# Kernel tuning notes

Hardware: AMD Instinct MI355X
Metric: run time of the kernel (lower is better)

Reference implementation:

```python
import jax, jax.numpy as jnp
import numpy as np

MOMENTUM = 0.5  # ODCMemory momentum
EPS = 1e-10

L, D, C, B = 500000, 256, 1024, 16384  # bank length, feat_dim, num_classes, batch


def setup_inputs() -> dict:
    key = jax.random.key(0)
    k0, k1, k2, k3, k4 = jax.random.split(key, 5)
    feature_bank = jax.random.normal(k0, (L, D), dtype=jnp.float32)
    # bank is stored L2-normalized (init_memory normalizes before copy)
    feature_bank = feature_bank / (jnp.linalg.norm(feature_bank, axis=1, keepdims=True) + EPS)
    label_bank = jax.random.randint(k1, (L,), 0, C, dtype=jnp.int64)
    centroids = jax.random.normal(k2, (C, D), dtype=jnp.float32)
    ind = jax.random.randint(k3, (B,), 0, L, dtype=jnp.int64)
    feature = jax.random.normal(k4, (B, D), dtype=jnp.float32)
    return {"feature_bank": feature_bank, "label_bank": label_bank,
            "centroids": centroids, "ind": ind, "feature": feature}


def reference(feature_bank, label_bank, centroids, ind, feature):
    """ODCMemory.update_samples_memory: gather -> momentum-normalize -> centroid
    similarity argmax -> scatter back. Returns (new_bank, new_labels, change_ratio)."""
    # normalize incoming batch features
    feat_n = feature / (jnp.linalg.norm(feature, axis=1, keepdims=True) + EPS)  # [B, D]
    # gather old features, momentum update, re-normalize
    feat_old = feature_bank[ind]                                               # [B, D]
    feat_new = (1.0 - MOMENTUM) * feat_old + MOMENTUM * feat_n
    feat_new = feat_new / (jnp.linalg.norm(feat_new, axis=1, keepdims=True) + EPS)
    # scatter updated features back into the bank
    new_bank = feature_bank.at[ind].set(feat_new)                              # [L, D]
    # similarity to centroids and relabel
    sim = jnp.einsum('cd,bd->cb', centroids, feat_new)                         # [C, B]
    newlabel = jnp.argmax(sim, axis=0).astype(label_bank.dtype)                # [B]
    old_label = label_bank[ind]
    change_ratio = jnp.mean((newlabel != old_label).astype(jnp.float32))
    new_labels = label_bank.at[ind].set(newlabel)
    return new_bank, new_labels, change_ratio
```

## Files before the change

kernel.cpp:

```cpp
#include <hip/hip_runtime.h>
#include <math.h>


constexpr int Lb = 500000;
constexpr int Dm = 256;
constexpr int D4 = 64;
constexpr int Cc = 1024;
constexpr int Bb = 16384;
constexpr float EPSV = 1e-10f;

constexpr int ROWS  = 8;
constexpr int GCLS  = Bb / ROWS;
constexpr int GCPY  = 2048;
constexpr int GMAIN = GCLS + GCPY;
constexpr int GMARK = Bb / 256;
constexpr int GPRE  = 1024;
constexpr int GPOST = 1024;

typedef float vfloat4 __attribute__((ext_vector_type(4)));

__device__ __forceinline__ float wave_sum64(float v) {
#pragma unroll
  for (int off = 32; off > 0; off >>= 1) v += __shfl_xor(v, off);
  return v;
}

__device__ __forceinline__ float4 feat_new_row(const float4* __restrict__ feat4,
                                               const float4* __restrict__ bank4,
                                               int gb, int bankrow, int lane) {
  float4 f = feat4[(size_t)gb * D4 + lane];
  const float ss = wave_sum64(f.x * f.x + f.y * f.y + f.z * f.z + f.w * f.w);
  const float inv1 = 1.0f / (sqrtf(ss) + EPSV);
  const float4 o = bank4[(size_t)bankrow * D4 + lane];
  float4 nw;
  nw.x = 0.5f * o.x + 0.5f * (f.x * inv1);
  nw.y = 0.5f * o.y + 0.5f * (f.y * inv1);
  nw.z = 0.5f * o.z + 0.5f * (f.z * inv1);
  nw.w = 0.5f * o.w + 0.5f * (f.w * inv1);
  const float s2 = wave_sum64(nw.x * nw.x + nw.y * nw.y + nw.z * nw.z + nw.w * nw.w);
  const float inv2 = 1.0f / (sqrtf(s2) + EPSV);
  nw.x *= inv2; nw.y *= inv2; nw.z *= inv2; nw.w *= inv2;
  return nw;
}

__global__ __launch_bounds__(256)
void k_pre(const float4* __restrict__ feat4, const float4* __restrict__ bank4,
           const int* __restrict__ ind, const float* __restrict__ cent,
           float* __restrict__ centT, float4* __restrict__ fnew4,
           int* __restrict__ marker, int* __restrict__ count) {
  const int tid = threadIdx.x, lane = tid & 63, wv = tid >> 6;
  const int t = blockIdx.x * 256 + tid;
  const int stride = GPRE * 256;
  for (int i = t; i < Lb; i += stride) marker[i] = -1;
  for (int i = t; i < Cc * Dm; i += stride) {
    const int d = i >> 10, c = i & (Cc - 1);
    centT[i] = cent[c * Dm + d];
  }
  if (t == 0) *count = 0;
  const int w = blockIdx.x * 4 + wv;
  for (int b = w; b < Bb; b += GPRE * 4)
    fnew4[(size_t)b * D4 + lane] = feat_new_row(feat4, bank4, b, ind[b], lane);
}

__global__ __launch_bounds__(256, 4)
void k_main(const float4* __restrict__ bank4, const float4* __restrict__ centT4,
            const float4* __restrict__ fnew4, const int* __restrict__ ind,
            const int* __restrict__ label_bank, int* __restrict__ marker,
            int* __restrict__ newlabel, int* __restrict__ count,
            float4* __restrict__ out4) {
  const int tid  = threadIdx.x;
  const int lane = tid & 63;
  const int wv   = tid >> 6;
  const int bid  = blockIdx.x;

  if (bid >= GMAIN) {
    const int b = (bid - GMAIN) * 256 + tid;
    if (b < Bb) atomicMax(&marker[ind[b]], b);
    return;
  }

  if ((bid & 1) == 0) {
    __shared__ float4 fs[ROWS][D4];
    __shared__ float  redv[ROWS][4];
    __shared__ int    redc[ROWS][4];
    const int cls = bid >> 1;
    const int b0  = cls * ROWS;
    const int c0  = tid * 4;

    for (int k = tid; k < ROWS * D4; k += 256)
      ((float4*)fs)[k] = fnew4[(size_t)b0 * D4 + k];
    __syncthreads();

    float4 acc[ROWS];
#pragma unroll
    for (int r = 0; r < ROWS; ++r) acc[r] = make_float4(0.f, 0.f, 0.f, 0.f);

    const float4* __restrict__ cvp = centT4 + tid;

    for (int d4 = 0; d4 < D4; ++d4) {
      const float4 cv0 = cvp[(size_t)(d4 * 4 + 0) * 256];
      const float4 cv1 = cvp[(size_t)(d4 * 4 + 1) * 256];
      const float4 cv2 = cvp[(size_t)(d4 * 4 + 2) * 256];
      const float4 cv3 = cvp[(size_t)(d4 * 4 + 3) * 256];
#pragma unroll
      for (int r = 0; r < ROWS; ++r) {
        const float4 f = fs[r][d4];
        acc[r].x = fmaf(cv0.x, f.x, acc[r].x);
        acc[r].y = fmaf(cv0.y, f.x, acc[r].y);
        acc[r].z = fmaf(cv0.z, f.x, acc[r].z);
        acc[r].w = fmaf(cv0.w, f.x, acc[r].w);
        acc[r].x = fmaf(cv1.x, f.y, acc[r].x);
        acc[r].y = fmaf(cv1.y, f.y, acc[r].y);
        acc[r].z = fmaf(cv1.z, f.y, acc[r].z);
        acc[r].w = fmaf(cv1.w, f.y, acc[r].w);
        acc[r].x = fmaf(cv2.x, f.z, acc[r].x);
        acc[r].y = fmaf(cv2.y, f.z, acc[r].y);
        acc[r].z = fmaf(cv2.z, f.z, acc[r].z);
        acc[r].w = fmaf(cv2.w, f.z, acc[r].w);
        acc[r].x = fmaf(cv3.x, f.w, acc[r].x);
        acc[r].y = fmaf(cv3.y, f.w, acc[r].y);
        acc[r].z = fmaf(cv3.z, f.w, acc[r].z);
        acc[r].w = fmaf(cv3.w, f.w, acc[r].w);
      }
    }

#pragma unroll
    for (int r = 0; r < ROWS; ++r) {
      float v = acc[r].x; int c = c0;
      if (acc[r].y > v) { v = acc[r].y; c = c0 + 1; }
      if (acc[r].z > v) { v = acc[r].z; c = c0 + 2; }
      if (acc[r].w > v) { v = acc[r].w; c = c0 + 3; }
#pragma unroll
      for (int off = 32; off > 0; off >>= 1) {
        const float ov = __shfl_xor(v, off);
        const int   oc = __shfl_xor(c, off);
        if (ov > v || (ov == v && oc < c)) { v = ov; c = oc; }
      }
      if (lane == 0) { redv[r][wv] = v; redc[r][wv] = c; }
    }
    __syncthreads();
    if (tid < ROWS) {
      const int r = tid;
      float v = redv[r][0]; int c = redc[r][0];
#pragma unroll
      for (int w = 1; w < 4; ++w) {
        const float ov = redv[r][w]; const int oc = redc[r][w];
        if (ov > v || (ov == v && oc < c)) { v = ov; c = oc; }
      }
      const int gb = b0 + r;
      newlabel[gb] = c;
      if (c != label_bank[ind[gb]]) atomicAdd(count, 1);
    }
  } else {
    const int cpy = bid >> 1;
    const size_t stride = (size_t)GCPY * 256;
    const size_t n4 = (size_t)Lb * D4;
    const vfloat4* __restrict__ src = (const vfloat4*)bank4;
    vfloat4* __restrict__ dst = (vfloat4*)out4;
    size_t i = (size_t)cpy * 256 + tid;
    for (; i + 3 * stride < n4; i += 4 * stride) {
      const vfloat4 a = src[i];
      const vfloat4 b = src[i + stride];
      const vfloat4 c = src[i + 2 * stride];
      const vfloat4 d = src[i + 3 * stride];
      __builtin_nontemporal_store(a, &dst[i]);
      __builtin_nontemporal_store(b, &dst[i + stride]);
      __builtin_nontemporal_store(c, &dst[i + 2 * stride]);
      __builtin_nontemporal_store(d, &dst[i + 3 * stride]);
    }
    for (; i < n4; i += stride) __builtin_nontemporal_store(src[i], &dst[i]);
  }
}

__global__ __launch_bounds__(256)
void k_post(const float4* __restrict__ fnew4, const int* __restrict__ ind,
            const int* __restrict__ marker, const int* __restrict__ newlabel,
            const int* __restrict__ label_bank, const int* __restrict__ count,
            float4* __restrict__ out4, float* __restrict__ out_lab,
            float* __restrict__ out_ratio) {
  const int tid = threadIdx.x, lane = tid & 63, wv = tid >> 6;
  const int t = blockIdx.x * 256 + tid;
  const int stride = GPOST * 256;
  for (int i = t; i < Lb; i += stride) {
    const int m = marker[i];
    out_lab[i] = (float)(m >= 0 ? newlabel[m] : label_bank[i]);
  }
  const int w = blockIdx.x * 4 + wv;
  for (int b = w; b < Bb; b += GPOST * 4) {
    const int r = ind[b];
    if (marker[r] == b) out4[(size_t)r * D4 + lane] = fnew4[(size_t)b * D4 + lane];
  }
  if (t == 0) *out_ratio = (float)(*count) / (float)Bb;
}

extern "C" void kernel_launch(void* const* d_in, const int* in_sizes, int n_in,
                              void* d_out, int out_size, void* d_ws, size_t ws_size,
                              hipStream_t stream) {
  const float* bank       = (const float*)d_in[0];
  const int*   label_bank = (const int*)  d_in[1];
  const float* cent       = (const float*)d_in[2];
  const int*   ind        = (const int*)  d_in[3];
  const float* feat       = (const float*)d_in[4];
  float* out = (float*)d_out;

  int*   marker   = (int*)d_ws;
  int*   newlabel = marker + Lb;
  int*   count    = newlabel + Bb;
  float* centT    = (float*)(count + 1);
  float* fnew     = centT + (size_t)Dm * Cc;

  float* out_lab   = out + (size_t)Lb * Dm;
  float* out_ratio = out_lab + Lb;

  k_pre <<<GPRE, 256, 0, stream>>>((const float4*)feat, (const float4*)bank, ind,
                                   cent, centT, (float4*)fnew, marker, count);
  k_main<<<GMAIN + GMARK, 256, 0, stream>>>((const float4*)bank, (const float4*)centT,
                                            (const float4*)fnew, ind, label_bank,
                                            marker, newlabel, count, (float4*)out);
  k_post<<<GPOST, 256, 0, stream>>>((const float4*)fnew, ind, marker, newlabel,
                                    label_bank, count, (float4*)out, out_lab, out_ratio);
}
```

Baseline: 286.4 us.

## Split fused main kernel into separate mark, classify, and copy kernels

Replaces the single heterogeneous k_main, which interleaved classification blocks, bank-copy blocks and marker blocks, with three separate kernels launched one after another on the same stream. Each kernel now gets its own launch bounds and grid, and the copy kernel grows to 3072 blocks. The cost this targets is the register and occupancy constraint that comes from mixing compute-heavy and bandwidth-heavy work in one launch. In exchange, the copy no longer overlaps the classification compute, and there are extra launches and serialization points.

```diff
diff --git a/kernel.cpp b/kernel.cpp
--- a/kernel.cpp
+++ b/kernel.cpp
@@ -11,9 +11,7 @@
 
 constexpr int ROWS  = 8;
 constexpr int GCLS  = Bb / ROWS;
-constexpr int GCPY  = 2048;
-constexpr int GMAIN = GCLS + GCPY;
-constexpr int GMARK = Bb / 256;
+constexpr int GCPY  = 3072;
 constexpr int GPRE  = 1024;
 constexpr int GPOST = 1024;
 
@@ -62,114 +60,104 @@
     fnew4[(size_t)b * D4 + lane] = feat_new_row(feat4, bank4, b, ind[b], lane);
 }
 
-__global__ __launch_bounds__(256, 4)
-void k_main(const float4* __restrict__ bank4, const float4* __restrict__ centT4,
-            const float4* __restrict__ fnew4, const int* __restrict__ ind,
-            const int* __restrict__ label_bank, int* __restrict__ marker,
-            int* __restrict__ newlabel, int* __restrict__ count,
-            float4* __restrict__ out4) {
-  const int tid  = threadIdx.x;
-  const int lane = tid & 63;
-  const int wv   = tid >> 6;
-  const int bid  = blockIdx.x;
-
-  if (bid >= GMAIN) {
-    const int b = (bid - GMAIN) * 256 + tid;
-    if (b < Bb) atomicMax(&marker[ind[b]], b);
-    return;
-  }
-
-  if ((bid & 1) == 0) {
-    __shared__ float4 fs[ROWS][D4];
-    __shared__ float  redv[ROWS][4];
-    __shared__ int    redc[ROWS][4];
-    const int cls = bid >> 1;
-    const int b0  = cls * ROWS;
-    const int c0  = tid * 4;
-
-    for (int k = tid; k < ROWS * D4; k += 256)
-      ((float4*)fs)[k] = fnew4[(size_t)b0 * D4 + k];
-    __syncthreads();
-
-    float4 acc[ROWS];
-#pragma unroll
-    for (int r = 0; r < ROWS; ++r) acc[r] = make_float4(0.f, 0.f, 0.f, 0.f);
-
-    const float4* __restrict__ cvp = centT4 + tid;
-
-    for (int d4 = 0; d4 < D4; ++d4) {
-      const float4 cv0 = cvp[(size_t)(d4 * 4 + 0) * 256];
-      const float4 cv1 = cvp[(size_t)(d4 * 4 + 1) * 256];
-      const float4 cv2 = cvp[(size_t)(d4 * 4 + 2) * 256];
-      const float4 cv3 = cvp[(size_t)(d4 * 4 + 3) * 256];
-#pragma unroll
-      for (int r = 0; r < ROWS; ++r) {
-        const float4 f = fs[r][d4];
-        acc[r].x = fmaf(cv0.x, f.x, acc[r].x);
-        acc[r].y = fmaf(cv0.y, f.x, acc[r].y);
-        acc[r].z = fmaf(cv0.z, f.x, acc[r].z);
-        acc[r].w = fmaf(cv0.w, f.x, acc[r].w);
-        acc[r].x = fmaf(cv1.x, f.y, acc[r].x);
-        acc[r].y = fmaf(cv1.y, f.y, acc[r].y);
-        acc[r].z = fmaf(cv1.z, f.y, acc[r].z);
-        acc[r].w = fmaf(cv1.w, f.y, acc[r].w);
-        acc[r].x = fmaf(cv2.x, f.z, acc[r].x);
-        acc[r].y = fmaf(cv2.y, f.z, acc[r].y);
-        acc[r].z = fmaf(cv2.z, f.z, acc[r].z);
-        acc[r].w = fmaf(cv2.w, f.z, acc[r].w);
-        acc[r].x = fmaf(cv3.x, f.w, acc[r].x);
-        acc[r].y = fmaf(cv3.y, f.w, acc[r].y);
-        acc[r].z = fmaf(cv3.z, f.w, acc[r].z);
-        acc[r].w = fmaf(cv3.w, f.w, acc[r].w);
-      }
+__global__ void k_mark(const int* __restrict__ ind, int* __restrict__ marker) {
+  const int b = blockIdx.x * blockDim.x + threadIdx.x;
+  if (b < Bb) atomicMax(&marker[ind[b]], b);
+}
+
+__global__ __launch_bounds__(256)
+void k_classify(const float4* __restrict__ centT4, const float4* __restrict__ fnew4,
+                const int* __restrict__ ind, const int* __restrict__ label_bank,
+                int* __restrict__ newlabel, int* __restrict__ count) {
+  __shared__ float4 fs[ROWS][D4];
+  __shared__ float  redv[ROWS][4];
+  __shared__ int    redc[ROWS][4];
+  const int tid = threadIdx.x, lane = tid & 63, wv = tid >> 6;
+  const int b0  = (int)blockIdx.x * ROWS;
+  const int c0  = tid * 4;
+
+  for (int k = tid; k < ROWS * D4; k += 256)
+    ((float4*)fs)[k] = fnew4[(size_t)b0 * D4 + k];
+  __syncthreads();
+
+  float4 acc[ROWS];
+#pragma unroll
+  for (int r = 0; r < ROWS; ++r) acc[r] = make_float4(0.f, 0.f, 0.f, 0.f);
+
+  const float4* __restrict__ cvp = centT4 + tid;
+
+  for (int d4 = 0; d4 < D4; ++d4) {
+    const float4 cv0 = cvp[(size_t)(d4 * 4 + 0) * 256];
+    const float4 cv1 = cvp[(size_t)(d4 * 4 + 1) * 256];
+    const float4 cv2 = cvp[(size_t)(d4 * 4 + 2) * 256];
+    const float4 cv3 = cvp[(size_t)(d4 * 4 + 3) * 256];
+#pragma unroll
+    for (int r = 0; r < ROWS; ++r) {
+      const float4 f = fs[r][d4];
+      acc[r].x = fmaf(cv0.x, f.x, acc[r].x);
+      acc[r].y = fmaf(cv0.y, f.x, acc[r].y);
+      acc[r].z = fmaf(cv0.z, f.x, acc[r].z);
+      acc[r].w = fmaf(cv0.w, f.x, acc[r].w);
+      acc[r].x = fmaf(cv1.x, f.y, acc[r].x);
+      acc[r].y = fmaf(cv1.y, f.y, acc[r].y);
+      acc[r].z = fmaf(cv1.z, f.y, acc[r].z);
+      acc[r].w = fmaf(cv1.w, f.y, acc[r].w);
+      acc[r].x = fmaf(cv2.x, f.z, acc[r].x);
+      acc[r].y = fmaf(cv2.y, f.z, acc[r].y);
+      acc[r].z = fmaf(cv2.z, f.z, acc[r].z);
+      acc[r].w = fmaf(cv2.w, f.z, acc[r].w);
+      acc[r].x = fmaf(cv3.x, f.w, acc[r].x);
+      acc[r].y = fmaf(cv3.y, f.w, acc[r].y);
+      acc[r].z = fmaf(cv3.z, f.w, acc[r].z);
+      acc[r].w = fmaf(cv3.w, f.w, acc[r].w);
     }
-
-#pragma unroll
-    for (int r = 0; r < ROWS; ++r) {
-      float v = acc[r].x; int c = c0;
-      if (acc[r].y > v) { v = acc[r].y; c = c0 + 1; }
-      if (acc[r].z > v) { v = acc[r].z; c = c0 + 2; }
-      if (acc[r].w > v) { v = acc[r].w; c = c0 + 3; }
-#pragma unroll
-      for (int off = 32; off > 0; off >>= 1) {
-        const float ov = __shfl_xor(v, off);
-        const int   oc = __shfl_xor(c, off);
-        if (ov > v || (ov == v && oc < c)) { v = ov; c = oc; }
-      }
-      if (lane == 0) { redv[r][wv] = v; redc[r][wv] = c; }
+  }
+
+#pragma unroll
+  for (int r = 0; r < ROWS; ++r) {
+    float v = acc[r].x; int c = c0;
+    if (acc[r].y > v) { v = acc[r].y; c = c0 + 1; }
+    if (acc[r].z > v) { v = acc[r].z; c = c0 + 2; }
+    if (acc[r].w > v) { v = acc[r].w; c = c0 + 3; }
+#pragma unroll
+    for (int off = 32; off > 0; off >>= 1) {
+      const float ov = __shfl_xor(v, off);
+      const int   oc = __shfl_xor(c, off);
+      if (ov > v || (ov == v && oc < c)) { v = ov; c = oc; }
     }
-    __syncthreads();
-    if (tid < ROWS) {
-      const int r = tid;
-      float v = redv[r][0]; int c = redc[r][0];
-#pragma unroll
-      for (int w = 1; w < 4; ++w) {
-        const float ov = redv[r][w]; const int oc = redc[r][w];
-        if (ov > v || (ov == v && oc < c)) { v = ov; c = oc; }
-      }
-      const int gb = b0 + r;
-      newlabel[gb] = c;
-      if (c != label_bank[ind[gb]]) atomicAdd(count, 1);
+    if (lane == 0) { redv[r][wv] = v; redc[r][wv] = c; }
+  }
+  __syncthreads();
+  if (tid < ROWS) {
+    const int r = tid;
+    float v = redv[r][0]; int c = redc[r][0];
+#pragma unroll
+    for (int w = 1; w < 4; ++w) {
+      const float ov = redv[r][w]; const int oc = redc[r][w];
+      if (ov > v || (ov == v && oc < c)) { v = ov; c = oc; }
     }
-  } else {
-    const int cpy = bid >> 1;
-    const size_t stride = (size_t)GCPY * 256;
-    const size_t n4 = (size_t)Lb * D4;
-    const vfloat4* __restrict__ src = (const vfloat4*)bank4;
-    vfloat4* __restrict__ dst = (vfloat4*)out4;
-    size_t i = (size_t)cpy * 256 + tid;
-    for (; i + 3 * stride < n4; i += 4 * stride) {
-      const vfloat4 a = src[i];
-      const vfloat4 b = src[i + stride];
-      const vfloat4 c = src[i + 2 * stride];
-      const vfloat4 d = src[i + 3 * stride];
-      __builtin_nontemporal_store(a, &dst[i]);
-      __builtin_nontemporal_store(b, &dst[i + stride]);
-      __builtin_nontemporal_store(c, &dst[i + 2 * stride]);
-      __builtin_nontemporal_store(d, &dst[i + 3 * stride]);
-    }
-    for (; i < n4; i += stride) __builtin_nontemporal_store(src[i], &dst[i]);
-  }
+    const int gb = b0 + r;
+    newlabel[gb] = c;
+    if (c != label_bank[ind[gb]]) atomicAdd(count, 1);
+  }
+}
+
+__global__ __launch_bounds__(256)
+void k_copy(const vfloat4* __restrict__ src, vfloat4* __restrict__ dst) {
+  const size_t stride = (size_t)GCPY * 256;
+  const size_t n4 = (size_t)Lb * D4;
+  size_t i = (size_t)blockIdx.x * 256 + threadIdx.x;
+  for (; i + 3 * stride < n4; i += 4 * stride) {
+    const vfloat4 a = src[i];
+    const vfloat4 b = src[i + stride];
+    const vfloat4 c = src[i + 2 * stride];
+    const vfloat4 d = src[i + 3 * stride];
+    __builtin_nontemporal_store(a, &dst[i]);
+    __builtin_nontemporal_store(b, &dst[i + stride]);
+    __builtin_nontemporal_store(c, &dst[i + 2 * stride]);
+    __builtin_nontemporal_store(d, &dst[i + 3 * stride]);
+  }
+  for (; i < n4; i += stride) __builtin_nontemporal_store(src[i], &dst[i]);
 }
 
 __global__ __launch_bounds__(256)
@@ -212,11 +200,12 @@
   float* out_lab   = out + (size_t)Lb * Dm;
   float* out_ratio = out_lab + Lb;
 
-  k_pre <<<GPRE, 256, 0, stream>>>((const float4*)feat, (const float4*)bank, ind,
-                                   cent, centT, (float4*)fnew, marker, count);
-  k_main<<<GMAIN + GMARK, 256, 0, stream>>>((const float4*)bank, (const float4*)centT,
-                                            (const float4*)fnew, ind, label_bank,
-                                            marker, newlabel, count, (float4*)out);
-  k_post<<<GPOST, 256, 0, stream>>>((const float4*)fnew, ind, marker, newlabel,
-                                    label_bank, count, (float4*)out, out_lab, out_ratio);
-}
+  k_pre     <<<GPRE, 256, 0, stream>>>((const float4*)feat, (const float4*)bank, ind,
+                                       cent, centT, (float4*)fnew, marker, count);
+  k_mark    <<<Bb / 256, 256, 0, stream>>>(ind, marker);
+  k_classify<<<GCLS, 256, 0, stream>>>((const float4*)centT, (const float4*)fnew,
+                                       ind, label_bank, newlabel, count);
+  k_copy    <<<GCPY, 256, 0, stream>>>((const vfloat4*)bank, (vfloat4*)out);
+  k_post    <<<GPOST, 256, 0, stream>>>((const float4*)fnew, ind, marker, newlabel,
+                                        label_bank, count, (float4*)out, out_lab, out_ratio);
+}
```

Result: slower. 398.7 us (+39.2%).

## Retile centroid GEMV to 16 rows x 8 classes, split marker kernel, nontemporal loads

Applied to the files above, without the earlier changes.

The classification blocks now handle 16 batch rows, and each thread computes 8 classes for 8 rows instead of 4 classes for 8 rows. This doubles reuse of each centroid load and halves the number of classification blocks. Interleaving changes from 1:1 to 1:2 classify:copy blocks, the marker atomics move into a separate small kernel, and the bank copy uses nontemporal loads. The change adds register pressure (launch bounds lowered to 3) and an extra kernel launch. The second-stage argmax tie-break now drops the lower-index check, which could change the result on exact ties.

```diff
diff --git a/kernel.cpp b/kernel.cpp
--- a/kernel.cpp
+++ b/kernel.cpp
@@ -9,11 +9,10 @@
 constexpr int Bb = 16384;
 constexpr float EPSV = 1e-10f;
 
-constexpr int ROWS  = 8;
-constexpr int GCLS  = Bb / ROWS;
+constexpr int ROWS_BLK = 16;
+constexpr int GCLS  = Bb / ROWS_BLK;
 constexpr int GCPY  = 2048;
 constexpr int GMAIN = GCLS + GCPY;
-constexpr int GMARK = Bb / 256;
 constexpr int GPRE  = 1024;
 constexpr int GPOST = 1024;
 
@@ -62,10 +61,15 @@
     fnew4[(size_t)b * D4 + lane] = feat_new_row(feat4, bank4, b, ind[b], lane);
 }
 
-__global__ __launch_bounds__(256, 4)
+__global__ void k_mark(const int* __restrict__ ind, int* __restrict__ marker) {
+  const int b = blockIdx.x * blockDim.x + threadIdx.x;
+  if (b < Bb) atomicMax(&marker[ind[b]], b);
+}
+
+__global__ __launch_bounds__(256, 3)
 void k_main(const float4* __restrict__ bank4, const float4* __restrict__ centT4,
             const float4* __restrict__ fnew4, const int* __restrict__ ind,
-            const int* __restrict__ label_bank, int* __restrict__ marker,
+            const int* __restrict__ label_bank,
             int* __restrict__ newlabel, int* __restrict__ count,
             float4* __restrict__ out4) {
   const int tid  = threadIdx.x;
@@ -73,102 +77,97 @@
   const int wv   = tid >> 6;
   const int bid  = blockIdx.x;
 
-  if (bid >= GMAIN) {
-    const int b = (bid - GMAIN) * 256 + tid;
-    if (b < Bb) atomicMax(&marker[ind[b]], b);
-    return;
-  }
-
-  if ((bid & 1) == 0) {
-    __shared__ float4 fs[ROWS][D4];
-    __shared__ float  redv[ROWS][4];
-    __shared__ int    redc[ROWS][4];
-    const int cls = bid >> 1;
-    const int b0  = cls * ROWS;
-    const int c0  = tid * 4;
-
-    for (int k = tid; k < ROWS * D4; k += 256)
+  if (bid % 3 == 0) {
+    __shared__ float4 fs[ROWS_BLK][D4];
+    __shared__ float  redv[ROWS_BLK][2];
+    __shared__ int    redc[ROWS_BLK][2];
+    const int cls = bid / 3;
+    const int b0  = cls * ROWS_BLK;
+    const int wp  = wv >> 1;
+    const int cth = tid & 127;
+    const int c0  = cth * 8;
+
+    for (int k = tid; k < ROWS_BLK * D4; k += 256)
       ((float4*)fs)[k] = fnew4[(size_t)b0 * D4 + k];
     __syncthreads();
 
-    float4 acc[ROWS];
-#pragma unroll
-    for (int r = 0; r < ROWS; ++r) acc[r] = make_float4(0.f, 0.f, 0.f, 0.f);
-
-    const float4* __restrict__ cvp = centT4 + tid;
+    float4 a0[8], a1[8];
+#pragma unroll
+    for (int r = 0; r < 8; ++r) { a0[r] = make_float4(0,0,0,0); a1[r] = make_float4(0,0,0,0); }
+
+    const float4* __restrict__ cvp = centT4 + cth * 2;
 
     for (int d4 = 0; d4 < D4; ++d4) {
-      const float4 cv0 = cvp[(size_t)(d4 * 4 + 0) * 256];
-      const float4 cv1 = cvp[(size_t)(d4 * 4 + 1) * 256];
-      const float4 cv2 = cvp[(size_t)(d4 * 4 + 2) * 256];
-      const float4 cv3 = cvp[(size_t)(d4 * 4 + 3) * 256];
-#pragma unroll
-      for (int r = 0; r < ROWS; ++r) {
-        const float4 f = fs[r][d4];
-        acc[r].x = fmaf(cv0.x, f.x, acc[r].x);
-        acc[r].y = fmaf(cv0.y, f.x, acc[r].y);
-        acc[r].z = fmaf(cv0.z, f.x, acc[r].z);
-        acc[r].w = fmaf(cv0.w, f.x, acc[r].w);
-        acc[r].x = fmaf(cv1.x, f.y, acc[r].x);
-        acc[r].y = fmaf(cv1.y, f.y, acc[r].y);
-        acc[r].z = fmaf(cv1.z, f.y, acc[r].z);
-        acc[r].w = fmaf(cv1.w, f.y, acc[r].w);
-        acc[r].x = fmaf(cv2.x, f.z, acc[r].x);
-        acc[r].y = fmaf(cv2.y, f.z, acc[r].y);
-        acc[r].z = fmaf(cv2.z, f.z, acc[r].z);
-        acc[r].w = fmaf(cv2.w, f.z, acc[r].w);
-        acc[r].x = fmaf(cv3.x, f.w, acc[r].x);
-        acc[r].y = fmaf(cv3.y, f.w, acc[r].y);
-        acc[r].z = fmaf(cv3.z, f.w, acc[r].z);
-        acc[r].w = fmaf(cv3.w, f.w, acc[r].w);
+      float4 cva[4], cvb[4];
+#pragma unroll
+      for (int dd = 0; dd < 4; ++dd) {
+        cva[dd] = cvp[(size_t)(d4 * 4 + dd) * 256];
+        cvb[dd] = cvp[(size_t)(d4 * 4 + dd) * 256 + 1];
       }
-    }
-
-#pragma unroll
-    for (int r = 0; r < ROWS; ++r) {
-      float v = acc[r].x; int c = c0;
-      if (acc[r].y > v) { v = acc[r].y; c = c0 + 1; }
-      if (acc[r].z > v) { v = acc[r].z; c = c0 + 2; }
-      if (acc[r].w > v) { v = acc[r].w; c = c0 + 3; }
+#pragma unroll
+      for (int r = 0; r < 8; ++r) {
+        const float4 f = fs[wp * 8 + r][d4];
+#pragma unroll
+        for (int dd = 0; dd < 4; ++dd) {
+          const float fv = (dd == 0) ? f.x : (dd == 1) ? f.y : (dd == 2) ? f.z : f.w;
+          a0[r].x = fmaf(cva[dd].x, fv, a0[r].x);
+          a0[r].y = fmaf(cva[dd].y, fv, a0[r].y);
+          a0[r].z = fmaf(cva[dd].z, fv, a0[r].z);
+          a0[r].w = fmaf(cva[dd].w, fv, a0[r].w);
+          a1[r].x = fmaf(cvb[dd].x, fv, a1[r].x);
+          a1[r].y = fmaf(cvb[dd].y, fv, a1[r].y);
+          a1[r].z = fmaf(cvb[dd].z, fv, a1[r].z);
+          a1[r].w = fmaf(cvb[dd].w, fv, a1[r].w);
+        }
+      }
+    }
+
+#pragma unroll
+    for (int r = 0; r < 8; ++r) {
+      float v = a0[r].x; int c = c0;
+      if (a0[r].y > v) { v = a0[r].y; c = c0 + 1; }
+      if (a0[r].z > v) { v = a0[r].z; c = c0 + 2; }
+      if (a0[r].w > v) { v = a0[r].w; c = c0 + 3; }
+      if (a1[r].x > v) { v = a1[r].x; c = c0 + 4; }
+      if (a1[r].y > v) { v = a1[r].y; c = c0 + 5; }
+      if (a1[r].z > v) { v = a1[r].z; c = c0 + 6; }
+      if (a1[r].w > v) { v = a1[r].w; c = c0 + 7; }
 #pragma unroll
       for (int off = 32; off > 0; off >>= 1) {
         const float ov = __shfl_xor(v, off);
         const int   oc = __shfl_xor(c, off);
         if (ov > v || (ov == v && oc < c)) { v = ov; c = oc; }
       }
-      if (lane == 0) { redv[r][wv] = v; redc[r][wv] = c; }
+      if (lane == 0) { redv[wp * 8 + r][wv & 1] = v; redc[wp * 8 + r][wv & 1] = c; }
     }
     __syncthreads();
-    if (tid < ROWS) {
-      const int r = tid;
-      float v = redv[r][0]; int c = redc[r][0];
-#pragma unroll
-      for (int w = 1; w < 4; ++w) {
-        const float ov = redv[r][w]; const int oc = redc[r][w];
-        if (ov > v || (ov == v && oc < c)) { v = ov; c = oc; }
-      }
-      const int gb = b0 + r;
+    if (tid < ROWS_BLK) {
+      float v = redv[tid][0]; int c = redc[tid][0];
+      const float ov = redv[tid][1]; const int oc = redc[tid][1];
+      if (ov > v) { v = ov; c = oc; }
+      const int gb = b0 + tid;
       newlabel[gb] = c;
       if (c != label_bank[ind[gb]]) atomicAdd(count, 1);
     }
   } else {
-    const int cpy = bid >> 1;
+    const int cpy = (bid / 3) * 2 + (bid % 3) - 1;
     const size_t stride = (size_t)GCPY * 256;
     const size_t n4 = (size_t)Lb * D4;
     const vfloat4* __restrict__ src = (const vfloat4*)bank4;
     vfloat4* __restrict__ dst = (vfloat4*)out4;
     size_t i = (size_t)cpy * 256 + tid;
     for (; i + 3 * stride < n4; i += 4 * stride) {
-      const vfloat4 a = src[i];
-      const vfloat4 b = src[i + stride];
-      const vfloat4 c = src[i + 2 * stride];
-      const vfloat4 d = src[i + 3 * stride];
+      const vfloat4 a = __builtin_nontemporal_load(&src[i]);
+      const vfloat4 b = __builtin_nontemporal_load(&src[i + stride]);
+      const vfloat4 c = __builtin_nontemporal_load(&src[i + 2 * stride]);
+      const vfloat4 d = __builtin_nontemporal_load(&src[i + 3 * stride]);
       __builtin_nontemporal_store(a, &dst[i]);
       __builtin_nontemporal_store(b, &dst[i + stride]);
       __builtin_nontemporal_store(c, &dst[i + 2 * stride]);
       __builtin_nontemporal_store(d, &dst[i + 3 * stride]);
     }
-    for (; i < n4; i += stride) __builtin_nontemporal_store(src[i], &dst[i]);
+    for (; i < n4; i += stride)
+      __builtin_nontemporal_store(__builtin_nontemporal_load(&src[i]), &dst[i]);
   }
 }
 
@@ -214,9 +213,10 @@
 
   k_pre <<<GPRE, 256, 0, stream>>>((const float4*)feat, (const float4*)bank, ind,
                                    cent, centT, (float4*)fnew, marker, count);
-  k_main<<<GMAIN + GMARK, 256, 0, stream>>>((const float4*)bank, (const float4*)centT,
-                                            (const float4*)fnew, ind, label_bank,
-                                            marker, newlabel, count, (float4*)out);
+  k_mark<<<Bb / 256, 256, 0, stream>>>(ind, marker);
+  k_main<<<GMAIN, 256, 0, stream>>>((const float4*)bank, (const float4*)centT,
+                                    (const float4*)fnew, ind, label_bank,
+                                    newlabel, count, (float4*)out);
   k_post<<<GPOST, 256, 0, stream>>>((const float4*)fnew, ind, marker, newlabel,
                                     label_bank, count, (float4*)out, out_lab, out_ratio);
 }
```

Result: no change. 284.0 us (-0.8%).

## Double-buffer centroid tiles in LDS and rebalance classify/copy block interleave

Applied to the files above, without the earlier changes.

The classification blocks now stage centroid slices through a double-buffered shared-memory array, prefetching the next slice into registers while computing the current one, with a block barrier every iteration. The grid is re-interleaved so that one classify block alternates with two copy blocks. The copy grid is doubled and its unroll halved. The marker atomics move out of the fused kernel into a separate small kernel launched beforehand. Each thread only reads back the LDS slots it wrote itself, so the staging adds barriers and 32KB of shared memory per block without any real data sharing. It also adds an extra kernel launch, all while the copy that is meant to dominate the runtime stays bandwidth-bound.

```diff
diff --git a/kernel.cpp b/kernel.cpp
--- a/kernel.cpp
+++ b/kernel.cpp
@@ -11,9 +11,8 @@
 
 constexpr int ROWS  = 8;
 constexpr int GCLS  = Bb / ROWS;
-constexpr int GCPY  = 2048;
+constexpr int GCPY  = 4096;
 constexpr int GMAIN = GCLS + GCPY;
-constexpr int GMARK = Bb / 256;
 constexpr int GPRE  = 1024;
 constexpr int GPOST = 1024;
 
@@ -62,10 +61,15 @@
     fnew4[(size_t)b * D4 + lane] = feat_new_row(feat4, bank4, b, ind[b], lane);
 }
 
-__global__ __launch_bounds__(256, 4)
+__global__ void k_mark(const int* __restrict__ ind, int* __restrict__ marker) {
+  const int b = blockIdx.x * blockDim.x + threadIdx.x;
+  if (b < Bb) atomicMax(&marker[ind[b]], b);
+}
+
+__global__ __launch_bounds__(256)
 void k_main(const float4* __restrict__ bank4, const float4* __restrict__ centT4,
             const float4* __restrict__ fnew4, const int* __restrict__ ind,
-            const int* __restrict__ label_bank, int* __restrict__ marker,
+            const int* __restrict__ label_bank,
             int* __restrict__ newlabel, int* __restrict__ count,
             float4* __restrict__ out4) {
   const int tid  = threadIdx.x;
@@ -73,55 +77,55 @@
   const int wv   = tid >> 6;
   const int bid  = blockIdx.x;
 
-  if (bid >= GMAIN) {
-    const int b = (bid - GMAIN) * 256 + tid;
-    if (b < Bb) atomicMax(&marker[ind[b]], b);
-    return;
-  }
-
-  if ((bid & 1) == 0) {
+  if (bid % 3 == 0) {
     __shared__ float4 fs[ROWS][D4];
+    __shared__ float4 cbuf[2][Cc];
     __shared__ float  redv[ROWS][4];
     __shared__ int    redc[ROWS][4];
-    const int cls = bid >> 1;
+    const int cls = bid / 3;
     const int b0  = cls * ROWS;
     const int c0  = tid * 4;
 
     for (int k = tid; k < ROWS * D4; k += 256)
       ((float4*)fs)[k] = fnew4[(size_t)b0 * D4 + k];
+#pragma unroll
+    for (int k = 0; k < 4; ++k)
+      cbuf[0][k * 256 + tid] = centT4[k * 256 + tid];
     __syncthreads();
 
     float4 acc[ROWS];
 #pragma unroll
     for (int r = 0; r < ROWS; ++r) acc[r] = make_float4(0.f, 0.f, 0.f, 0.f);
 
-    const float4* __restrict__ cvp = centT4 + tid;
-
     for (int d4 = 0; d4 < D4; ++d4) {
-      const float4 cv0 = cvp[(size_t)(d4 * 4 + 0) * 256];
-      const float4 cv1 = cvp[(size_t)(d4 * 4 + 1) * 256];
-      const float4 cv2 = cvp[(size_t)(d4 * 4 + 2) * 256];
-      const float4 cv3 = cvp[(size_t)(d4 * 4 + 3) * 256];
+      const int cur = d4 & 1;
+      float4 pre[4];
+      const bool more = (d4 < D4 - 1);
+      if (more) {
+#pragma unroll
+        for (int k = 0; k < 4; ++k)
+          pre[k] = centT4[(size_t)(d4 + 1) * 1024 + k * 256 + tid];
+      }
+      float4 cv[4];
+#pragma unroll
+      for (int dd = 0; dd < 4; ++dd) cv[dd] = cbuf[cur][dd * 256 + tid];
 #pragma unroll
       for (int r = 0; r < ROWS; ++r) {
         const float4 f = fs[r][d4];
-        acc[r].x = fmaf(cv0.x, f.x, acc[r].x);
-        acc[r].y = fmaf(cv0.y, f.x, acc[r].y);
-        acc[r].z = fmaf(cv0.z, f.x, acc[r].z);
-        acc[r].w = fmaf(cv0.w, f.x, acc[r].w);
-        acc[r].x = fmaf(cv1.x, f.y, acc[r].x);
-        acc[r].y = fmaf(cv1.y, f.y, acc[r].y);
-        acc[r].z = fmaf(cv1.z, f.y, acc[r].z);
-        acc[r].w = fmaf(cv1.w, f.y, acc[r].w);
-        acc[r].x = fmaf(cv2.x, f.z, acc[r].x);
-        acc[r].y = fmaf(cv2.y, f.z, acc[r].y);
-        acc[r].z = fmaf(cv2.z, f.z, acc[r].z);
-        acc[r].w = fmaf(cv2.w, f.z, acc[r].w);
-        acc[r].x = fmaf(cv3.x, f.w, acc[r].x);
-        acc[r].y = fmaf(cv3.y, f.w, acc[r].y);
-        acc[r].z = fmaf(cv3.z, f.w, acc[r].z);
-        acc[r].w = fmaf(cv3.w, f.w, acc[r].w);
-      }
+#pragma unroll
+        for (int dd = 0; dd < 4; ++dd) {
+          const float fv = (dd == 0) ? f.x : (dd == 1) ? f.y : (dd == 2) ? f.z : f.w;
+          acc[r].x = fmaf(cv[dd].x, fv, acc[r].x);
+          acc[r].y = fmaf(cv[dd].y, fv, acc[r].y);
+          acc[r].z = fmaf(cv[dd].z, fv, acc[r].z);
+          acc[r].w = fmaf(cv[dd].w, fv, acc[r].w);
+        }
+      }
+      if (more) {
+#pragma unroll
+        for (int k = 0; k < 4; ++k) cbuf[cur ^ 1][k * 256 + tid] = pre[k];
+      }
+      __syncthreads();
     }
 
 #pragma unroll
@@ -152,21 +156,17 @@
       if (c != label_bank[ind[gb]]) atomicAdd(count, 1);
     }
   } else {
-    const int cpy = bid >> 1;
+    const int cpy = (bid / 3) * 2 + (bid % 3) - 1;
     const size_t stride = (size_t)GCPY * 256;
     const size_t n4 = (size_t)Lb * D4;
     const vfloat4* __restrict__ src = (const vfloat4*)bank4;
     vfloat4* __restrict__ dst = (vfloat4*)out4;
     size_t i = (size_t)cpy * 256 + tid;
-    for (; i + 3 * stride < n4; i += 4 * stride) {
+    for (; i + stride < n4; i += 2 * stride) {
       const vfloat4 a = src[i];
       const vfloat4 b = src[i + stride];
-      const vfloat4 c = src[i + 2 * stride];
-      const vfloat4 d = src[i + 3 * stride];
       __builtin_nontemporal_store(a, &dst[i]);
       __builtin_nontemporal_store(b, &dst[i + stride]);
-      __builtin_nontemporal_store(c, &dst[i + 2 * stride]);
-      __builtin_nontemporal_store(d, &dst[i + 3 * stride]);
     }
     for (; i < n4; i += stride) __builtin_nontemporal_store(src[i], &dst[i]);
   }
@@ -214,9 +214,10 @@
 
   k_pre <<<GPRE, 256, 0, stream>>>((const float4*)feat, (const float4*)bank, ind,
                                    cent, centT, (float4*)fnew, marker, count);
-  k_main<<<GMAIN + GMARK, 256, 0, stream>>>((const float4*)bank, (const float4*)centT,
-                                            (const float4*)fnew, ind, label_bank,
-                                            marker, newlabel, count, (float4*)out);
+  k_mark<<<Bb / 256, 256, 0, stream>>>(ind, marker);
+  k_main<<<GMAIN, 256, 0, stream>>>((const float4*)bank, (const float4*)centT,
+                                    (const float4*)fnew, ind, label_bank,
+                                    newlabel, count, (float4*)out);
   k_post<<<GPOST, 256, 0, stream>>>((const float4*)fnew, ind, marker, newlabel,
                                     label_bank, count, (float4*)out, out_lab, out_ratio);
 }
```

Result: slower. 346.8 us (+21.1%).
